# Kernel optimization log

Hardware: AMD Instinct MI355X
Metric: run time of the kernel (lower is better)

Reference implementation:

```python
import jax, jax.numpy as jnp
import numpy as np

DIM = 512
HEADS = 8
HEAD_DIM = DIM // HEADS
SCALE = HEAD_DIM ** -0.5
EPS = 1e-5


def setup_inputs() -> dict:
    key = jax.random.key(0)
    ks = jax.random.split(key, 6)
    B, N, C = 4, 2048, DIM
    x = jax.random.normal(ks[0], (B, N, C), dtype=jnp.float32)
    w_qkv = jax.random.normal(ks[1], (C, 3 * C), dtype=jnp.float32) * (C ** -0.5)
    w_proj = jax.random.normal(ks[2], (C, C), dtype=jnp.float32) * (C ** -0.5)
    b_proj = jax.random.normal(ks[3], (C,), dtype=jnp.float32) * 0.02
    gamma = jnp.ones((C,), dtype=jnp.float32)
    beta = jnp.zeros((C,), dtype=jnp.float32)
    return {"x": x, "w_qkv": w_qkv, "w_proj": w_proj, "b_proj": b_proj,
            "gamma": gamma, "beta": beta}


def reference(x, w_qkv, w_proj, b_proj, gamma, beta):
    B, N, C = x.shape
    # LayerNorm over channel dim
    mu = jnp.mean(x, axis=-1, keepdims=True)
    var = jnp.mean(jnp.square(x - mu), axis=-1, keepdims=True)
    xn = (x - mu) * jax.lax.rsqrt(var + EPS) * gamma + beta
    # QKV projection (fp32, no bias)
    qkv = xn @ w_qkv  # [B, N, 3C]
    qkv = qkv.reshape(B, N, 3, HEADS, HEAD_DIM)
    q = jnp.transpose(qkv[:, :, 0], (0, 2, 1, 3))  # [B, H, N, D]
    k = jnp.transpose(qkv[:, :, 1], (0, 2, 1, 3))
    v = jnp.transpose(qkv[:, :, 2], (0, 2, 1, 3))
    attn = jnp.einsum('bhnd,bhmd->bhnm', q, k) * SCALE
    attn = jax.nn.softmax(attn, axis=-1)
    out = jnp.einsum('bhnm,bhmd->bhnd', attn, v)  # [B, H, N, D]
    out = jnp.transpose(out, (0, 2, 1, 3)).reshape(B, N, C)
    out = out @ w_proj + b_proj
    return x + out
```

## Files before the change

### kernel.cpp

```cpp
#include <hip/hip_runtime.h>
#include <hip/hip_bf16.h>
#include <math.h>

typedef _Float16 f16;
typedef _Float16 half8 __attribute__((ext_vector_type(8)));
typedef _Float16 half4 __attribute__((ext_vector_type(4)));
typedef float f32x4 __attribute__((ext_vector_type(4)));

#define DIMC 512
#define HEADS 8
#define HD 64
#define BB 4
#define NN 2048
#define MM (BB*NN)
#define NQKV (3*DIMC)
#define SCALE 0.125f
#define LOG2E 1.44269504f
#define EPSLN 1e-5f
#define NCHUNK 4

__device__ __forceinline__ void g2l16(const void* g, void* l) {
    __builtin_amdgcn_global_load_lds(
        (const __attribute__((address_space(1))) unsigned int*)g,
        (__attribute__((address_space(3))) unsigned int*)l, 16, 0, 0);
}

__global__ __launch_bounds__(256) void ln_kernel(const float* __restrict__ x,
                                                 const float* __restrict__ gamma,
                                                 const float* __restrict__ beta,
                                                 f16* __restrict__ xn) {
    int w = threadIdx.x >> 6;
    int lane = threadIdx.x & 63;
    int row = blockIdx.x * 4 + w;
    const float* xr = x + (size_t)row * DIMC;
    float4 v0 = ((const float4*)xr)[lane * 2];
    float4 v1 = ((const float4*)xr)[lane * 2 + 1];
    float s = v0.x + v0.y + v0.z + v0.w + v1.x + v1.y + v1.z + v1.w;
#pragma unroll
    for (int off = 1; off < 64; off <<= 1) s += __shfl_xor(s, off);
    float mu = s * (1.0f / DIMC);
    float d0 = v0.x - mu, d1 = v0.y - mu, d2 = v0.z - mu, d3 = v0.w - mu;
    float d4 = v1.x - mu, d5 = v1.y - mu, d6 = v1.z - mu, d7 = v1.w - mu;
    float s2 = d0*d0 + d1*d1 + d2*d2 + d3*d3 + d4*d4 + d5*d5 + d6*d6 + d7*d7;
#pragma unroll
    for (int off = 1; off < 64; off <<= 1) s2 += __shfl_xor(s2, off);
    float rstd = rsqrtf(s2 * (1.0f / DIMC) + EPSLN);
    float4 g0 = ((const float4*)gamma)[lane * 2];
    float4 g1 = ((const float4*)gamma)[lane * 2 + 1];
    float4 b0 = ((const float4*)beta)[lane * 2];
    float4 b1 = ((const float4*)beta)[lane * 2 + 1];
    half8 o;
    o[0] = (f16)(d0 * rstd * g0.x + b0.x);
    o[1] = (f16)(d1 * rstd * g0.y + b0.y);
    o[2] = (f16)(d2 * rstd * g0.z + b0.z);
    o[3] = (f16)(d3 * rstd * g0.w + b0.w);
    o[4] = (f16)(d4 * rstd * g1.x + b1.x);
    o[5] = (f16)(d5 * rstd * g1.y + b1.y);
    o[6] = (f16)(d6 * rstd * g1.z + b1.z);
    o[7] = (f16)(d7 * rstd * g1.w + b1.w);
    ((half8*)(xn + (size_t)row * DIMC))[lane] = o;
}

__global__ __launch_bounds__(256) void transpose_cast(const float* __restrict__ src,
                                                      f16* __restrict__ dst,
                                                      int R, int C) {
    __shared__ f16 t[32][72];
    int k0 = blockIdx.y * 32, n0 = blockIdx.x * 64;
    int tid = threadIdx.x;
    int rr = tid >> 6, col = tid & 63;
#pragma unroll
    for (int p = 0; p < 8; p++) {
        int r = p * 4 + rr;
        t[r][col] = (f16)src[(size_t)(k0 + r) * C + n0 + col];
    }
    __syncthreads();
    int nl = tid >> 2, kc = (tid & 3) * 8;
    half8 v;
#pragma unroll
    for (int j = 0; j < 8; j++) v[j] = t[kc + j][nl];
    *(half8*)&dst[(size_t)(n0 + nl) * R + k0 + kc] = v;
}

__device__ __forceinline__ void gemm128_loop(const char* Ag, const char* Bg,
                                             f16* As, f16* Bs, f32x4 (&acc)[4][4]) {
    int tid = threadIdx.x;
    int w = tid >> 6, lane = tid & 63, l15 = lane & 15, quad = lane >> 4;
    int wy = w >> 1, wx = w & 1;
    int off0 = w * 1024 + lane * 16;
    for (int kk = 0; kk < 16; ++kk) {
        __syncthreads();
#pragma unroll
        for (int c = 0; c < 2; ++c) {
            int off = c * 4096 + off0;
            int row = off >> 6, col = off & 63;
            g2l16(Ag + (size_t)row * 1024 + kk * 64 + col, (char*)As + c * 4096 + w * 1024);
            g2l16(Bg + (size_t)row * 1024 + kk * 64 + col, (char*)Bs + c * 4096 + w * 1024);
        }
        __syncthreads();
        half8 af[4], bf[4];
#pragma unroll
        for (int i = 0; i < 4; ++i) {
            af[i] = *(const half8*)((const char*)As + ((wy * 64 + i * 16 + l15) << 6) + quad * 16);
            bf[i] = *(const half8*)((const char*)Bs + ((wx * 64 + i * 16 + l15) << 6) + quad * 16);
        }
#pragma unroll
        for (int i = 0; i < 4; ++i)
#pragma unroll
            for (int j = 0; j < 4; ++j)
                acc[i][j] = __builtin_amdgcn_mfma_f32_16x16x32_f16(af[i], bf[j], acc[i][j], 0, 0, 0);
    }
}

__global__ __launch_bounds__(256) void gemm_qkv(const f16* __restrict__ xn,
                                                const f16* __restrict__ wt,
                                                f16* __restrict__ qb,
                                                f16* __restrict__ kbuf,
                                                f16* __restrict__ vtb) {
    __shared__ __align__(16) f16 As[128 * 32];
    __shared__ __align__(16) f16 Bs[128 * 32];
    int tid = threadIdx.x;
    int w = tid >> 6, lane = tid & 63, l15 = lane & 15, quad = lane >> 4;
    int wy = w >> 1, wx = w & 1;
    int m0 = blockIdx.y * 128, c0 = blockIdx.x * 128;
    f32x4 acc[4][4] = {};
    gemm128_loop((const char*)(xn + (size_t)m0 * DIMC),
                 (const char*)(wt + (size_t)c0 * DIMC), As, Bs, acc);
    int bx = blockIdx.x;
    if (bx < 8) {
        const float QS = SCALE * LOG2E;
        f16* dst = (bx < 4) ? qb : kbuf;
        float mul = (bx < 4) ? QS : 1.0f;
        int cb = (bx < 4) ? c0 : c0 - DIMC;
#pragma unroll
        for (int i = 0; i < 4; ++i)
#pragma unroll
            for (int j = 0; j < 4; ++j)
#pragma unroll
                for (int r = 0; r < 4; ++r) {
                    int m = m0 + wy * 64 + i * 16 + quad * 4 + r;
                    int c = cb + wx * 64 + j * 16 + l15;
                    int b = m >> 11, n = m & 2047;
                    int h = c >> 6, d = c & 63;
                    dst[(((size_t)(b * HEADS + h)) * NN + n) * HD + d] = (f16)(acc[i][j][r] * mul);
                }
    } else {
        __syncthreads();
        f16* T = (f16*)As + w * 512;
        int cb = c0 - 2 * DIMC;
        int dl = lane >> 2, mp = lane & 3;
#pragma unroll
        for (int i = 0; i < 4; ++i)
#pragma unroll
            for (int j = 0; j < 4; ++j) {
                half4 hv;
#pragma unroll
                for (int r = 0; r < 4; ++r) hv[r] = (f16)acc[i][j][r];
                *(half4*)&T[l15 * 20 + quad * 4] = hv;
                half4 rv = *(half4*)&T[dl * 20 + mp * 4];
                int c = cb + wx * 64 + j * 16 + dl;
                int m = m0 + wy * 64 + i * 16 + mp * 4;
                int b = m >> 11, n = m & 2047;
                int h = c >> 6, d = c & 63;
                *(half4*)&vtb[(((size_t)(b * HEADS + h)) * HD + d) * NN + n] = rv;
            }
    }
}

__global__ __launch_bounds__(256, 4) void attn_kernel(const f16* __restrict__ qb,
                                                      const f16* __restrict__ kbuf,
                                                      const f16* __restrict__ vtb,
                                                      f16* __restrict__ po,
                                                      float2* __restrict__ pml) {
    __shared__ __align__(16) f16 Ks[64 * 72];
    __shared__ __align__(16) f16 Vs[64 * 72];
    int bh = blockIdx.y;
    int chunk = blockIdx.z;
    int n0 = blockIdx.x * 128;
    int tid = threadIdx.x, w = tid >> 6, lane = tid & 63, l15 = lane & 15, quad = lane >> 4;
    const f16* Kbase = kbuf + (size_t)bh * NN * HD;
    const f16* Vbase = vtb + (size_t)bh * HD * NN;
    const f16* Qbase = qb + (size_t)bh * NN * HD;
    half8 qf[2][2];
#pragma unroll
    for (int qt = 0; qt < 2; ++qt) {
        const f16* qr = Qbase + (size_t)(n0 + w * 32 + qt * 16 + l15) * HD + quad * 8;
        qf[qt][0] = *(const half8*)qr;
        qf[qt][1] = *(const half8*)(qr + 32);
    }
    f32x4 ot[2][4] = {};
    float m_run[2] = {-INFINITY, -INFINITY};
    float l_run[2] = {0.f, 0.f};
    int srow = tid >> 2, part = (tid & 3) * 16;
    int kbeg = chunk * (NN / NCHUNK);
    half8 kp0, kp1, vp0, vp1;
    {
        const f16* kg = Kbase + (size_t)(kbeg + srow) * HD + part;
        kp0 = ((const half8*)kg)[0]; kp1 = ((const half8*)kg)[1];
        const f16* vg = Vbase + (size_t)srow * NN + kbeg + part;
        vp0 = ((const half8*)vg)[0]; vp1 = ((const half8*)vg)[1];
    }
    for (int it = 0; it < NN / NCHUNK / 64; ++it) {
        __syncthreads();
        *(half8*)&Ks[srow * 72 + part] = kp0;
        *(half8*)&Ks[srow * 72 + part + 8] = kp1;
        *(half8*)&Vs[srow * 72 + part] = vp0;
        *(half8*)&Vs[srow * 72 + part + 8] = vp1;
        __syncthreads();
        if (it < NN / NCHUNK / 64 - 1) {
            int kt0 = kbeg + (it + 1) * 64;
            const f16* kg = Kbase + (size_t)(kt0 + srow) * HD + part;
            kp0 = ((const half8*)kg)[0]; kp1 = ((const half8*)kg)[1];
            const f16* vg = Vbase + (size_t)srow * NN + kt0 + part;
            vp0 = ((const half8*)vg)[0]; vp1 = ((const half8*)vg)[1];
        }
        f32x4 s0[4], s1[4];
#pragma unroll
        for (int kt = 0; kt < 4; ++kt) {
            half8 a0 = *(const half8*)&Ks[(kt * 16 + l15) * 72 + quad * 8];
            half8 a1 = *(const half8*)&Ks[(kt * 16 + l15) * 72 + 32 + quad * 8];
            f32x4 z0 = {};
            z0 = __builtin_amdgcn_mfma_f32_16x16x32_f16(a0, qf[0][0], z0, 0, 0, 0);
            z0 = __builtin_amdgcn_mfma_f32_16x16x32_f16(a1, qf[0][1], z0, 0, 0, 0);
            s0[kt] = z0;
            f32x4 z1 = {};
            z1 = __builtin_amdgcn_mfma_f32_16x16x32_f16(a0, qf[1][0], z1, 0, 0, 0);
            z1 = __builtin_amdgcn_mfma_f32_16x16x32_f16(a1, qf[1][1], z1, 0, 0, 0);
            s1[kt] = z1;
        }
        half4 pb[2][4];
#pragma unroll
        for (int qt = 0; qt < 2; ++qt) {
            f32x4* s = (qt == 0) ? s0 : s1;
            float tmax = -INFINITY;
#pragma unroll
            for (int kt = 0; kt < 4; ++kt)
#pragma unroll
                for (int r = 0; r < 4; ++r) tmax = fmaxf(tmax, s[kt][r]);
            tmax = fmaxf(tmax, __shfl_xor(tmax, 16));
            tmax = fmaxf(tmax, __shfl_xor(tmax, 32));
            float m_new = fmaxf(m_run[qt], tmax);
            float alpha = __builtin_amdgcn_exp2f(m_run[qt] - m_new);
            m_run[qt] = m_new;
            float lsum = 0.f;
#pragma unroll
            for (int kt = 0; kt < 4; ++kt)
#pragma unroll
                for (int r = 0; r < 4; ++r) {
                    float p = __builtin_amdgcn_exp2f(s[kt][r] - m_new);
                    s[kt][r] = p;
                    lsum += p;
                }
            lsum += __shfl_xor(lsum, 16);
            lsum += __shfl_xor(lsum, 32);
            l_run[qt] = l_run[qt] * alpha + lsum;
#pragma unroll
            for (int dt = 0; dt < 4; ++dt)
#pragma unroll
                for (int r = 0; r < 4; ++r) ot[qt][dt][r] *= alpha;
#pragma unroll
            for (int kt = 0; kt < 4; ++kt) {
                half4 pk;
#pragma unroll
                for (int r = 0; r < 4; ++r) pk[r] = (f16)s[kt][r];
                pb[qt][kt] = pk;
            }
        }
#pragma unroll
        for (int kt = 0; kt < 4; ++kt)
#pragma unroll
            for (int dt = 0; dt < 4; ++dt) {
                half4 av = *(const half4*)&Vs[(dt * 16 + l15) * 72 + kt * 16 + quad * 4];
                ot[0][dt] = __builtin_amdgcn_mfma_f32_16x16x16f16(av, pb[0][kt], ot[0][dt], 0, 0, 0);
                ot[1][dt] = __builtin_amdgcn_mfma_f32_16x16x16f16(av, pb[1][kt], ot[1][dt], 0, 0, 0);
            }
    }
    size_t rowbase = ((size_t)chunk * (BB * HEADS) + bh) * NN;
#pragma unroll
    for (int qt = 0; qt < 2; ++qt) {
        int n = n0 + w * 32 + qt * 16 + l15;
        if (quad == 0) {
            float2 ml; ml.x = m_run[qt]; ml.y = l_run[qt];
            pml[rowbase + n] = ml;
        }
#pragma unroll
        for (int dt = 0; dt < 4; ++dt) {
            half4 hv;
#pragma unroll
            for (int r = 0; r < 4; ++r) hv[r] = (f16)ot[qt][dt][r];
            *(half4*)&po[(rowbase + n) * HD + dt * 16 + quad * 4] = hv;
        }
    }
}

__global__ __launch_bounds__(256) void attn_combine(const f16* __restrict__ po,
                                                    const float2* __restrict__ pml,
                                                    f16* __restrict__ ao) {
    int gid = blockIdx.x * 256 + threadIdx.x;
    int row = gid >> 3, d0 = (gid & 7) * 8;
    int bh = row >> 11, n = row & 2047;
    const int CS = BB * HEADS * NN;
    float2 ml[NCHUNK];
    float M = -INFINITY;
#pragma unroll
    for (int c = 0; c < NCHUNK; ++c) {
        ml[c] = pml[row + c * CS];
        M = fmaxf(M, ml[c].x);
    }
    float a[NCHUNK], denom = 0.f;
#pragma unroll
    for (int c = 0; c < NCHUNK; ++c) {
        a[c] = __builtin_amdgcn_exp2f(ml[c].x - M);
        denom += ml[c].y * a[c];
    }
    float inv = 1.0f / denom;
    float acc[8] = {};
#pragma unroll
    for (int c = 0; c < NCHUNK; ++c) {
        half8 oc = *(const half8*)&po[((size_t)row + c * CS) * HD + d0];
#pragma unroll
        for (int j = 0; j < 8; ++j) acc[j] += (float)oc[j] * a[c];
    }
    half8 r;
#pragma unroll
    for (int j = 0; j < 8; ++j) r[j] = (f16)(acc[j] * inv);
    int h = bh & 7, b = bh >> 3;
    *(half8*)&ao[((size_t)(b * NN + n)) * DIMC + h * HD + d0] = r;
}

__global__ __launch_bounds__(256) void gemm_proj(const f16* __restrict__ aob,
                                                 const f16* __restrict__ wt,
                                                 const float* __restrict__ x,
                                                 const float* __restrict__ bias,
                                                 float* __restrict__ out) {
    __shared__ __align__(16) f16 As[128 * 32];
    __shared__ __align__(16) f16 Bs[64 * 32];
    int tid = threadIdx.x;
    int w = tid >> 6, lane = tid & 63, l15 = lane & 15, quad = lane >> 4;
    int m0 = blockIdx.y * 128, c0 = blockIdx.x * 64;
    const char* Ag = (const char*)(aob + (size_t)m0 * DIMC);
    const char* Bg = (const char*)(wt + (size_t)c0 * DIMC);
    f32x4 acc[2][4] = {};
    int off0 = w * 1024 + lane * 16;
    for (int kk = 0; kk < 16; ++kk) {
        __syncthreads();
#pragma unroll
        for (int c = 0; c < 2; ++c) {
            int off = c * 4096 + off0;
            int row = off >> 6, col = off & 63;
            g2l16(Ag + (size_t)row * 1024 + kk * 64 + col, (char*)As + c * 4096 + w * 1024);
        }
        {
            int off = tid * 16;
            int row = off >> 6, col = off & 63;
            g2l16(Bg + (size_t)row * 1024 + kk * 64 + col, (char*)Bs + w * 1024);
        }
        __syncthreads();
        half8 af[2], bf[4];
#pragma unroll
        for (int i = 0; i < 2; ++i)
            af[i] = *(const half8*)((const char*)As + ((w * 32 + i * 16 + l15) << 6) + quad * 16);
#pragma unroll
        for (int j = 0; j < 4; ++j)
            bf[j] = *(const half8*)((const char*)Bs + ((j * 16 + l15) << 6) + quad * 16);
#pragma unroll
        for (int i = 0; i < 2; ++i)
#pragma unroll
            for (int j = 0; j < 4; ++j)
                acc[i][j] = __builtin_amdgcn_mfma_f32_16x16x32_f16(af[i], bf[j], acc[i][j], 0, 0, 0);
    }
#pragma unroll
    for (int i = 0; i < 2; ++i)
#pragma unroll
        for (int j = 0; j < 4; ++j)
#pragma unroll
            for (int r = 0; r < 4; ++r) {
                int m = m0 + w * 32 + i * 16 + quad * 4 + r;
                int c = c0 + j * 16 + l15;
                out[(size_t)m * DIMC + c] = x[(size_t)m * DIMC + c] + bias[c] + acc[i][j][r];
            }
}

extern "C" void kernel_launch(void* const* d_in, const int* in_sizes, int n_in,
                              void* d_out, int out_size, void* d_ws, size_t ws_size,
                              hipStream_t stream) {
    (void)in_sizes; (void)n_in; (void)out_size; (void)ws_size;
    const float* x     = (const float*)d_in[0];
    const float* wqkv  = (const float*)d_in[1];
    const float* wproj = (const float*)d_in[2];
    const float* bproj = (const float*)d_in[3];
    const float* gamma = (const float*)d_in[4];
    const float* beta  = (const float*)d_in[5];
    float* out = (float*)d_out;

    char* ws = (char*)d_ws;
    f16* xn     = (f16*)ws;                 ws += (size_t)MM * DIMC * 2;
    f16* wqkvt  = (f16*)ws;                 ws += (size_t)NQKV * DIMC * 2;
    f16* wprojt = (f16*)ws;                 ws += (size_t)DIMC * DIMC * 2;
    f16* qbuf   = (f16*)ws;                 ws += (size_t)MM * DIMC * 2;
    f16* kbuf   = (f16*)ws;                 ws += (size_t)MM * DIMC * 2;
    f16* vtbuf  = (f16*)ws;                 ws += (size_t)MM * DIMC * 2;
    f16* aobuf  = (f16*)ws;                 ws += (size_t)MM * DIMC * 2;
    f16* po     = (f16*)ws;                 ws += (size_t)NCHUNK * BB * HEADS * NN * HD * 2;
    float2* pml = (float2*)ws;              ws += (size_t)NCHUNK * BB * HEADS * NN * sizeof(float2);

    ln_kernel<<<MM / 4, 256, 0, stream>>>(x, gamma, beta, xn);
    transpose_cast<<<dim3(NQKV / 64, DIMC / 32), 256, 0, stream>>>(wqkv, wqkvt, DIMC, NQKV);
    transpose_cast<<<dim3(DIMC / 64, DIMC / 32), 256, 0, stream>>>(wproj, wprojt, DIMC, DIMC);
    gemm_qkv<<<dim3(NQKV / 128, MM / 128), 256, 0, stream>>>(xn, wqkvt, qbuf, kbuf, vtbuf);
    attn_kernel<<<dim3(NN / 128, BB * HEADS, NCHUNK), 256, 0, stream>>>(qbuf, kbuf, vtbuf, po, pml);
    attn_combine<<<(BB * HEADS * NN * HD / 8) / 256, 256, 0, stream>>>(po, pml, aobuf);
    gemm_proj<<<dim3(DIMC / 64, MM / 128), 256, 0, stream>>>(aobuf, wprojt, x, bproj, out);
}
```

Baseline: 184.8 us.

## Register-prefetch next K tile in QKV and proj GEMMs instead of direct global-to-LDS loads

Both GEMM K loops now load the next K slice from global memory into registers while the MFMAs for the current slice run. At the top of each iteration those registers are stored to LDS. This replaces the synchronous global_load_lds path, whose load latency was exposed between the two barriers each iteration. The cost is more VGPRs and an extra VGPR-to-LDS store step.

```diff
diff --git a/kernel.cpp b/kernel.cpp
--- a/kernel.cpp
+++ b/kernel.cpp
@@ -18,12 +18,6 @@
 #define LOG2E 1.44269504f
 #define EPSLN 1e-5f
 #define NCHUNK 4
-
-__device__ __forceinline__ void g2l16(const void* g, void* l) {
-    __builtin_amdgcn_global_load_lds(
-        (const __attribute__((address_space(1))) unsigned int*)g,
-        (__attribute__((address_space(3))) unsigned int*)l, 16, 0, 0);
-}
 
 __global__ __launch_bounds__(256) void ln_kernel(const float* __restrict__ x,
                                                  const float* __restrict__ gamma,
@@ -87,16 +81,28 @@
     int w = tid >> 6, lane = tid & 63, l15 = lane & 15, quad = lane >> 4;
     int wy = w >> 1, wx = w & 1;
     int off0 = w * 1024 + lane * 16;
+    int offA0 = off0, offA1 = 4096 + off0;
+    int rA0 = offA0 >> 6, cA0 = offA0 & 63;
+    int rA1 = offA1 >> 6, cA1 = offA1 & 63;
+    half8 ar0, ar1, br0, br1;
+    ar0 = *(const half8*)(Ag + (size_t)rA0 * 1024 + cA0);
+    ar1 = *(const half8*)(Ag + (size_t)rA1 * 1024 + cA1);
+    br0 = *(const half8*)(Bg + (size_t)rA0 * 1024 + cA0);
+    br1 = *(const half8*)(Bg + (size_t)rA1 * 1024 + cA1);
     for (int kk = 0; kk < 16; ++kk) {
         __syncthreads();
-#pragma unroll
-        for (int c = 0; c < 2; ++c) {
-            int off = c * 4096 + off0;
-            int row = off >> 6, col = off & 63;
-            g2l16(Ag + (size_t)row * 1024 + kk * 64 + col, (char*)As + c * 4096 + w * 1024);
-            g2l16(Bg + (size_t)row * 1024 + kk * 64 + col, (char*)Bs + c * 4096 + w * 1024);
-        }
-        __syncthreads();
+        *(half8*)((char*)As + offA0) = ar0;
+        *(half8*)((char*)As + offA1) = ar1;
+        *(half8*)((char*)Bs + offA0) = br0;
+        *(half8*)((char*)Bs + offA1) = br1;
+        __syncthreads();
+        if (kk < 15) {
+            int ko = (kk + 1) * 64;
+            ar0 = *(const half8*)(Ag + (size_t)rA0 * 1024 + ko + cA0);
+            ar1 = *(const half8*)(Ag + (size_t)rA1 * 1024 + ko + cA1);
+            br0 = *(const half8*)(Bg + (size_t)rA0 * 1024 + ko + cA0);
+            br1 = *(const half8*)(Bg + (size_t)rA1 * 1024 + ko + cA1);
+        }
         half8 af[4], bf[4];
 #pragma unroll
         for (int i = 0; i < 4; ++i) {
@@ -341,20 +347,27 @@
     const char* Bg = (const char*)(wt + (size_t)c0 * DIMC);
     f32x4 acc[2][4] = {};
     int off0 = w * 1024 + lane * 16;
+    int offA1 = 4096 + off0;
+    int rA0 = off0 >> 6, cA0 = off0 & 63;
+    int rA1 = offA1 >> 6, cA1 = offA1 & 63;
+    int offB = tid * 16;
+    int rB = offB >> 6, cB = offB & 63;
+    half8 ar0, ar1, br0;
+    ar0 = *(const half8*)(Ag + (size_t)rA0 * 1024 + cA0);
+    ar1 = *(const half8*)(Ag + (size_t)rA1 * 1024 + cA1);
+    br0 = *(const half8*)(Bg + (size_t)rB * 1024 + cB);
     for (int kk = 0; kk < 16; ++kk) {
         __syncthreads();
-#pragma unroll
-        for (int c = 0; c < 2; ++c) {
-            int off = c * 4096 + off0;
-            int row = off >> 6, col = off & 63;
-            g2l16(Ag + (size_t)row * 1024 + kk * 64 + col, (char*)As + c * 4096 + w * 1024);
-        }
-        {
-            int off = tid * 16;
-            int row = off >> 6, col = off & 63;
-            g2l16(Bg + (size_t)row * 1024 + kk * 64 + col, (char*)Bs + w * 1024);
-        }
-        __syncthreads();
+        *(half8*)((char*)As + off0) = ar0;
+        *(half8*)((char*)As + offA1) = ar1;
+        *(half8*)((char*)Bs + offB) = br0;
+        __syncthreads();
+        if (kk < 15) {
+            int ko = (kk + 1) * 64;
+            ar0 = *(const half8*)(Ag + (size_t)rA0 * 1024 + ko + cA0);
+            ar1 = *(const half8*)(Ag + (size_t)rA1 * 1024 + ko + cA1);
+            br0 = *(const half8*)(Bg + (size_t)rB * 1024 + ko + cB);
+        }
         half8 af[2], bf[4];
 #pragma unroll
         for (int i = 0; i < 2; ++i)
```

New measurement: 192.1 us. 3.9% more time.
